# Kernel optimization log

Measured on AMD Instinct MI355X. Metric: run time of the kernel, lower is better.

## Reference

```python
import jax, jax.numpy as jnp
import numpy as np

T, B, D, H = 1024, 128, 256, 256


def setup_inputs() -> dict:
    key = jax.random.key(0)
    ks = jax.random.split(key, 16)
    s_in = 1.0 / np.sqrt(D + H)  # torch Linear default init scale
    inp = {
        "inputs": jax.random.normal(ks[0], (T, B, D), dtype=jnp.float32),
        "Wf": jax.random.uniform(ks[1], (H, D + H), jnp.float32, -s_in, s_in),
        "bf": jax.random.uniform(ks[2], (H,), jnp.float32, -s_in, s_in),
        "Wi": jax.random.uniform(ks[3], (H, D + H), jnp.float32, -s_in, s_in),
        "bi": jax.random.uniform(ks[4], (H,), jnp.float32, -s_in, s_in),
        "Wg": jax.random.uniform(ks[5], (H, D + H), jnp.float32, -s_in, s_in),
        "bg": jax.random.uniform(ks[6], (H,), jnp.float32, -s_in, s_in),
        "Wo": jax.random.uniform(ks[7], (H, D + H), jnp.float32, -s_in, s_in),
        "bo": jax.random.uniform(ks[8], (H,), jnp.float32, -s_in, s_in),
        # estimator params stacked over the 4 gates (order: f, i, g, o)
        "estW1": jax.random.uniform(ks[9], (4, 8, H), jnp.float32, -1/np.sqrt(H), 1/np.sqrt(H)),
        "estb1": jax.random.uniform(ks[10], (4, 8), jnp.float32, -1/np.sqrt(H), 1/np.sqrt(H)),
        "estW2": jax.random.uniform(ks[11], (4, 4, 8), jnp.float32, -1/np.sqrt(8), 1/np.sqrt(8)),
        "estb2": jax.random.uniform(ks[12], (4, 4), jnp.float32, -1/np.sqrt(8), 1/np.sqrt(8)),
        "estW3": jax.random.uniform(ks[13], (4, 1, 4), jnp.float32, -0.5, 0.5),
        "estb3": jax.random.uniform(ks[14], (4, 1), jnp.float32, -0.5, 0.5),
    }
    return inp


def reference(inputs, Wf, bf, Wi, bi, Wg, bg, Wo, bo,
              estW1, estb1, estW2, estb2, estW3, estb3):
    def est(x, k):
        # tiny MLP: H -> 8 -> 4 -> 1 with tanh/tanh/sigmoid
        h1 = jnp.tanh(x @ estW1[k].T + estb1[k])
        h2 = jnp.tanh(h1 @ estW2[k].T + estb2[k])
        return jax.nn.sigmoid(h2 @ estW3[k].T + estb3[k])  # [B, 1]

    def step(carry, x):
        hx, cx = carry
        comb = jnp.concatenate([x, hx], axis=1)  # [B, D+H]
        f = jax.nn.sigmoid(comb @ Wf.T + bf)
        i = jax.nn.sigmoid(comb @ Wi.T + bi)
        g = jnp.tanh(comb @ Wg.T + bg)
        o = jax.nn.sigmoid(comb @ Wo.T + bo)
        f = f * est(f, 0)
        i = i * est(i, 1)
        g = g * est(g, 2)
        o = o * est(o, 3)
        cx = f * cx + i * g
        hx = o * jnp.tanh(cx)
        return (hx, cx), hx

    hx0 = jnp.zeros((B, H), dtype=inputs.dtype)
    cx0 = jnp.zeros((B, H), dtype=inputs.dtype)
    (hx, cx), stacked = jax.lax.scan(step, (hx0, cx0), inputs)
    return stacked, hx, cx
```

## Files before the change

### kernel.cpp

```cpp
#include <hip/hip_runtime.h>
#include <hip/hip_fp16.h>
#include <math.h>

#define T_STEPS 1024
#define BATCH   128
#define D_IN    256
#define H_DIM   256
#define NCOL    1024
#define CH      16

typedef _Float16 half2_t __attribute__((ext_vector_type(2)));

__device__ __forceinline__ float sigmoidf_(float x) {
    return 1.0f / (1.0f + __expf(-x));
}

__device__ __forceinline__ float tanhf_(float x) {
    float ax = fabsf(x);
    float t = __expf(-2.0f * ax);
    float r = (1.0f - t) / (1.0f + t);
    return copysignf(r, x);
}

__device__ __forceinline__ float dot2f(unsigned int w, unsigned int h, float acc) {
#if __has_builtin(__builtin_amdgcn_fdot2)
    return __builtin_amdgcn_fdot2(__builtin_bit_cast(half2_t, w),
                                  __builtin_bit_cast(half2_t, h), acc, false);
#else
    __half2 wv = *(__half2*)&w, hv = *(__half2*)&h;
    acc = fmaf(__half2float(wv.x), __half2float(hv.x), acc);
    return fmaf(__half2float(wv.y), __half2float(hv.y), acc);
#endif
}

__device__ __forceinline__ unsigned int packh2(float a, float b) {
    __half2 p = __floats2half2_rn(a, b);
    return *(unsigned int*)&p;
}

__device__ __forceinline__ uint4 pack8(const float* p) {
    return make_uint4(packh2(p[0], p[1]), packh2(p[2], p[3]),
                      packh2(p[4], p[5]), packh2(p[6], p[7]));
}

__global__ __launch_bounds__(256) void prep_kernel(
    const float* __restrict__ Wf, const float* __restrict__ Wi,
    const float* __restrict__ Wg, const float* __restrict__ Wo,
    const float* __restrict__ bf, const float* __restrict__ bi,
    const float* __restrict__ bg, const float* __restrict__ bo,
    uint4* __restrict__ WX4, uint4* __restrict__ WH4,
    float* __restrict__ biasc)
{
    int idx = blockIdx.x * 256 + threadIdx.x;
    int m = idx >> 10;
    int j = idx & 1023;
    int g = j >> 8;
    int h = j & 255;
    const float* W = (g == 0) ? Wf : (g == 1) ? Wi : (g == 2) ? Wg : Wo;
    const float* row = W + h * (D_IN + H_DIM);
    WX4[idx] = pack8(row + 8 * m);
    WH4[idx] = pack8(row + D_IN + 8 * m);
    if (idx < NCOL) {
        const float* bb = (g == 0) ? bf : (g == 1) ? bi : (g == 2) ? bg : bo;
        biasc[idx] = bb[h];
    }
}

__global__ __launch_bounds__(1024) void qlstm_kernel(
    const float* __restrict__ x,
    const uint4* __restrict__ WX4,
    const uint4* __restrict__ WH4,
    const float* __restrict__ biasc,
    const float* __restrict__ estW1, const float* __restrict__ estb1,
    const float* __restrict__ estW2, const float* __restrict__ estb2,
    const float* __restrict__ estW3, const float* __restrict__ estb3,
    float* __restrict__ out)
{
    __shared__ __align__(16) __half hxh[H_DIM];
    __shared__ __align__(16) __half hxl[H_DIM];
    __shared__ __align__(16) float gact[NCOL];
    __shared__ float w1[4 * 8 * H_DIM];
    __shared__ float sb1[32];
    __shared__ float sW2[128];
    __shared__ float sb2[16];
    __shared__ float sW3[16];
    __shared__ float sb3[4];
    __shared__ float escale[4];

    const int b    = blockIdx.x;
    const int tid  = threadIdx.x;
    const int w    = tid >> 6;
    const int lane = tid & 63;

    for (int i = tid; i < 4 * 8 * H_DIM; i += 1024) {
        int p = i & 255;
        int base = i & ~255;
        int h = 4 * (p & 63) + (p >> 6);
        w1[i] = estW1[base + h];
    }
    if (tid < 32)  sb1[tid] = estb1[tid];
    if (tid < 128) sW2[tid] = estW2[tid];
    if (tid < 16)  { sb2[tid] = estb2[tid]; sW3[tid] = estW3[tid]; }
    if (tid < 4)   sb3[tid] = estb3[tid];
    if (tid < H_DIM) {
        hxh[tid] = __float2half(0.0f);
        hxl[tid] = __float2half(0.0f);
    }
    float c_reg = 0.0f, h_reg = 0.0f;
    const float b_j = biasc[tid];
    __syncthreads();

    const uint4* hh = (const uint4*)hxh;
    const uint4* hl = (const uint4*)hxl;

    float pacc[CH];

    for (int t0 = 0; t0 < T_STEPS; t0 += CH) {
        #pragma unroll
        for (int s = 0; s < CH; s++) pacc[s] = b_j;
        {
            const float* xb = x + ((size_t)t0 * BATCH + b) * D_IN;
            for (int m = 0; m < 32; m++) {
                uint4 wv = WX4[(m << 10) + tid];
                __half2 q0 = *(__half2*)&wv.x, q1 = *(__half2*)&wv.y;
                __half2 q2 = *(__half2*)&wv.z, q3 = *(__half2*)&wv.w;
                float w0 = __half2float(q0.x), w1f = __half2float(q0.y);
                float w2 = __half2float(q1.x), w3 = __half2float(q1.y);
                float w4 = __half2float(q2.x), w5 = __half2float(q2.y);
                float w6 = __half2float(q3.x), w7 = __half2float(q3.y);
                #pragma unroll
                for (int s = 0; s < CH; s++) {
                    const float* xr = xb + (size_t)s * (BATCH * D_IN) + (m << 3);
                    float4 xa = *(const float4*)xr;
                    float4 xc = *(const float4*)(xr + 4);
                    float a = pacc[s];
                    a = fmaf(w0, xa.x, a); a = fmaf(w1f, xa.y, a);
                    a = fmaf(w2, xa.z, a); a = fmaf(w3, xa.w, a);
                    a = fmaf(w4, xc.x, a); a = fmaf(w5, xc.y, a);
                    a = fmaf(w6, xc.z, a); a = fmaf(w7, xc.w, a);
                    pacc[s] = a;
                }
            }
        }

        #pragma unroll 1
        for (int s = 0; s < CH; s++) {
            const int t = t0 + s;
            float aH = pacc[s], aL = 0.0f;
            #pragma unroll 4
            for (int m = 0; m < 32; m++) {
                uint4 wv = WH4[(m << 10) + tid];
                uint4 hv = hh[m], lv = hl[m];
                aH = dot2f(wv.x, hv.x, aH); aH = dot2f(wv.y, hv.y, aH);
                aH = dot2f(wv.z, hv.z, aH); aH = dot2f(wv.w, hv.w, aH);
                aL = dot2f(wv.x, lv.x, aL); aL = dot2f(wv.y, lv.y, aL);
                aL = dot2f(wv.z, lv.z, aL); aL = dot2f(wv.w, lv.w, aL);
            }
            float acc = aH + aL;

            float v = (tid >= 512 && tid < 768) ? tanhf_(acc) : sigmoidf_(acc);
            gact[tid] = v;
            __syncthreads();

            if (tid < 256) {
                float4 gv = ((const float4*)(gact + (w << 8)))[lane];
                float h1[8];
                #pragma unroll
                for (int j = 0; j < 8; j++) {
                    const float* wr = &w1[(w * 8 + j) * H_DIM];
                    float sacc = fmaf(gv.x, wr[lane],
                                 fmaf(gv.y, wr[lane + 64],
                                 fmaf(gv.z, wr[lane + 128], gv.w * wr[lane + 192])));
                    #pragma unroll
                    for (int m2 = 1; m2 < 64; m2 <<= 1) sacc += __shfl_xor(sacc, m2, 64);
                    h1[j] = tanhf_(sacc + sb1[w * 8 + j]);
                }
                float h2[4];
                #pragma unroll
                for (int j = 0; j < 4; j++) {
                    float sacc = sb2[w * 4 + j];
                    #pragma unroll
                    for (int q = 0; q < 8; q++)
                        sacc = fmaf(h1[q], sW2[w * 32 + j * 8 + q], sacc);
                    h2[j] = tanhf_(sacc);
                }
                float s3 = sb3[w];
                #pragma unroll
                for (int q = 0; q < 4; q++) s3 = fmaf(h2[q], sW3[w * 4 + q], s3);
                if (lane == 0) escale[w] = sigmoidf_(s3);
            }
            __syncthreads();

            if (tid < 256) {
                float f  = gact[tid]       * escale[0];
                float ii = gact[256 + tid] * escale[1];
                float gg = gact[512 + tid] * escale[2];
                float o  = gact[768 + tid] * escale[3];
                c_reg = fmaf(f, c_reg, ii * gg);
                h_reg = o * tanhf_(c_reg);
                __half hi = __float2half_rn(h_reg);
                hxh[tid] = hi;
                hxl[tid] = __float2half_rn(h_reg - __half2float(hi));
                out[((size_t)t * BATCH + b) * H_DIM + tid] = h_reg;
            }
            __syncthreads();
        }
    }

    if (tid < 256) {
        const size_t stacked = (size_t)T_STEPS * BATCH * H_DIM;
        out[stacked + (size_t)b * H_DIM + tid] = h_reg;
        out[stacked + (size_t)BATCH * H_DIM + (size_t)b * H_DIM + tid] = c_reg;
    }
}

extern "C" void kernel_launch(void* const* d_in, const int* in_sizes, int n_in,
                              void* d_out, int out_size, void* d_ws, size_t ws_size,
                              hipStream_t stream) {
    const float* x     = (const float*)d_in[0];
    const float* Wf    = (const float*)d_in[1];
    const float* bf    = (const float*)d_in[2];
    const float* Wi    = (const float*)d_in[3];
    const float* bi    = (const float*)d_in[4];
    const float* Wg    = (const float*)d_in[5];
    const float* bg    = (const float*)d_in[6];
    const float* Wo    = (const float*)d_in[7];
    const float* bo    = (const float*)d_in[8];
    const float* estW1 = (const float*)d_in[9];
    const float* estb1 = (const float*)d_in[10];
    const float* estW2 = (const float*)d_in[11];
    const float* estb2 = (const float*)d_in[12];
    const float* estW3 = (const float*)d_in[13];
    const float* estb3 = (const float*)d_in[14];

    uint4* WX4   = (uint4*)d_ws;
    uint4* WH4   = WX4 + 32768;
    float* biasc = (float*)(WH4 + 32768);

    prep_kernel<<<128, 256, 0, stream>>>(Wf, Wi, Wg, Wo, bf, bi, bg, bo,
                                         WX4, WH4, biasc);
    qlstm_kernel<<<BATCH, 1024, 0, stream>>>(
        x, WX4, WH4, biasc,
        estW1, estb1, estW2, estb2, estW3, estb3, (float*)d_out);
}
```

Baseline: 10.64 ms.

## Keep part of recurrent weights in registers, prefetch the rest, spread estimator across waves

The first 8 of the 32 recurrent weight chunks per thread are now held in registers for the whole sequence. The remaining chunks are loaded in double-buffered groups of four, each issued ahead of the dot products that use it, to hide global-load latency on the serial recurrence path. The estimator's first layer is spread across all 16 waves (two hidden units per wave) instead of 4 waves. The small second and third layers are then recomputed redundantly by every thread that updates the cell. This raises register pressure, with launch bounds hinting 4 waves per SIMD, and adds redundant per-thread estimator math.

```diff
diff --git a/kernel.cpp b/kernel.cpp
--- a/kernel.cpp
+++ b/kernel.cpp
@@ -8,6 +8,7 @@
 #define H_DIM   256
 #define NCOL    1024
 #define CH      16
+#define NPER    8
 
 typedef _Float16 half2_t __attribute__((ext_vector_type(2)));
 
@@ -66,7 +67,16 @@
     }
 }
 
-__global__ __launch_bounds__(1024) void qlstm_kernel(
+#define DOT8(wv, mm)                                                        \
+    do {                                                                    \
+        uint4 hv_ = hh[mm], lv_ = hl[mm];                                   \
+        aH = dot2f((wv).x, hv_.x, aH); aH = dot2f((wv).y, hv_.y, aH);       \
+        aH = dot2f((wv).z, hv_.z, aH); aH = dot2f((wv).w, hv_.w, aH);       \
+        aL = dot2f((wv).x, lv_.x, aL); aL = dot2f((wv).y, lv_.y, aL);       \
+        aL = dot2f((wv).z, lv_.z, aL); aL = dot2f((wv).w, lv_.w, aL);       \
+    } while (0)
+
+__global__ __launch_bounds__(1024, 4) void qlstm_kernel(
     const float* __restrict__ x,
     const uint4* __restrict__ WX4,
     const uint4* __restrict__ WH4,
@@ -85,12 +95,14 @@
     __shared__ float sb2[16];
     __shared__ float sW3[16];
     __shared__ float sb3[4];
-    __shared__ float escale[4];
+    __shared__ float sh1[32];
 
     const int b    = blockIdx.x;
     const int tid  = threadIdx.x;
     const int w    = tid >> 6;
     const int lane = tid & 63;
+    const int g_e  = w >> 2;
+    const int j0   = (w & 3) * 2;
 
     for (int i = tid; i < 4 * 8 * H_DIM; i += 1024) {
         int p = i & 255;
@@ -112,6 +124,11 @@
 
     const uint4* hh = (const uint4*)hxh;
     const uint4* hl = (const uint4*)hxl;
+    const uint4* wcol = WH4 + tid;
+
+    uint4 wper[NPER];
+    #pragma unroll
+    for (int m = 0; m < NPER; m++) wper[m] = wcol[m << 10];
 
     float pacc[CH];
 
@@ -146,56 +163,84 @@
         #pragma unroll 1
         for (int s = 0; s < CH; s++) {
             const int t = t0 + s;
-            float aH = pacc[s], aL = 0.0f;
-            #pragma unroll 4
-            for (int m = 0; m < 32; m++) {
-                uint4 wv = WH4[(m << 10) + tid];
-                uint4 hv = hh[m], lv = hl[m];
-                aH = dot2f(wv.x, hv.x, aH); aH = dot2f(wv.y, hv.y, aH);
-                aH = dot2f(wv.z, hv.z, aH); aH = dot2f(wv.w, hv.w, aH);
-                aL = dot2f(wv.x, lv.x, aL); aL = dot2f(wv.y, lv.y, aL);
-                aL = dot2f(wv.z, lv.z, aL); aL = dot2f(wv.w, lv.w, aL);
-            }
+            float aH = pacc[0], aL = 0.0f;
+            #pragma unroll
+            for (int i = 0; i < CH - 1; i++) pacc[i] = pacc[i + 1];
+
+            uint4 sA[4], sB[4];
+            #pragma unroll
+            for (int i = 0; i < 4; i++) sA[i] = wcol[(NPER + i) << 10];
+            #pragma unroll
+            for (int i = 0; i < 4; i++) sB[i] = wcol[(NPER + 4 + i) << 10];
+
+            #pragma unroll
+            for (int m = 0; m < NPER; m++) DOT8(wper[m], m);
+
+            #pragma unroll
+            for (int i = 0; i < 4; i++) DOT8(sA[i], 8 + i);
+            #pragma unroll
+            for (int i = 0; i < 4; i++) sA[i] = wcol[(16 + i) << 10];
+            #pragma unroll
+            for (int i = 0; i < 4; i++) DOT8(sB[i], 12 + i);
+            #pragma unroll
+            for (int i = 0; i < 4; i++) sB[i] = wcol[(20 + i) << 10];
+            #pragma unroll
+            for (int i = 0; i < 4; i++) DOT8(sA[i], 16 + i);
+            #pragma unroll
+            for (int i = 0; i < 4; i++) sA[i] = wcol[(24 + i) << 10];
+            #pragma unroll
+            for (int i = 0; i < 4; i++) DOT8(sB[i], 20 + i);
+            #pragma unroll
+            for (int i = 0; i < 4; i++) sB[i] = wcol[(28 + i) << 10];
+            #pragma unroll
+            for (int i = 0; i < 4; i++) DOT8(sA[i], 24 + i);
+            #pragma unroll
+            for (int i = 0; i < 4; i++) DOT8(sB[i], 28 + i);
+
             float acc = aH + aL;
 
             float v = (tid >= 512 && tid < 768) ? tanhf_(acc) : sigmoidf_(acc);
             gact[tid] = v;
             __syncthreads();
 
-            if (tid < 256) {
-                float4 gv = ((const float4*)(gact + (w << 8)))[lane];
-                float h1[8];
+            {
+                float4 gv = ((const float4*)(gact + (g_e << 8)))[lane];
                 #pragma unroll
-                for (int j = 0; j < 8; j++) {
-                    const float* wr = &w1[(w * 8 + j) * H_DIM];
-                    float sacc = fmaf(gv.x, wr[lane],
-                                 fmaf(gv.y, wr[lane + 64],
-                                 fmaf(gv.z, wr[lane + 128], gv.w * wr[lane + 192])));
+                for (int jj = 0; jj < 2; jj++) {
+                    const int u = g_e * 8 + j0 + jj;
+                    const float* wr = &w1[u * H_DIM];
+                    float s1 = fmaf(gv.x, wr[lane],
+                               fmaf(gv.y, wr[lane + 64],
+                               fmaf(gv.z, wr[lane + 128], gv.w * wr[lane + 192])));
                     #pragma unroll
-                    for (int m2 = 1; m2 < 64; m2 <<= 1) sacc += __shfl_xor(sacc, m2, 64);
-                    h1[j] = tanhf_(sacc + sb1[w * 8 + j]);
+                    for (int m2 = 1; m2 < 64; m2 <<= 1) s1 += __shfl_xor(s1, m2, 64);
+                    if (lane == 0) sh1[u] = tanhf_(s1 + sb1[u]);
                 }
-                float h2[4];
-                #pragma unroll
-                for (int j = 0; j < 4; j++) {
-                    float sacc = sb2[w * 4 + j];
-                    #pragma unroll
-                    for (int q = 0; q < 8; q++)
-                        sacc = fmaf(h1[q], sW2[w * 32 + j * 8 + q], sacc);
-                    h2[j] = tanhf_(sacc);
-                }
-                float s3 = sb3[w];
-                #pragma unroll
-                for (int q = 0; q < 4; q++) s3 = fmaf(h2[q], sW3[w * 4 + q], s3);
-                if (lane == 0) escale[w] = sigmoidf_(s3);
             }
             __syncthreads();
 
             if (tid < 256) {
-                float f  = gact[tid]       * escale[0];
-                float ii = gact[256 + tid] * escale[1];
-                float gg = gact[512 + tid] * escale[2];
-                float o  = gact[768 + tid] * escale[3];
+                float esc[4];
+                #pragma unroll
+                for (int g = 0; g < 4; g++) {
+                    float h2[4];
+                    #pragma unroll
+                    for (int j = 0; j < 4; j++) {
+                        float s2 = sb2[g * 4 + j];
+                        #pragma unroll
+                        for (int q = 0; q < 8; q++)
+                            s2 = fmaf(sh1[g * 8 + q], sW2[g * 32 + j * 8 + q], s2);
+                        h2[j] = tanhf_(s2);
+                    }
+                    float s3 = sb3[g];
+                    #pragma unroll
+                    for (int q = 0; q < 4; q++) s3 = fmaf(h2[q], sW3[g * 4 + q], s3);
+                    esc[g] = sigmoidf_(s3);
+                }
+                float f  = gact[tid]       * esc[0];
+                float ii = gact[256 + tid] * esc[1];
+                float gg = gact[512 + tid] * esc[2];
+                float o  = gact[768 + tid] * esc[3];
                 c_reg = fmaf(f, c_reg, ii * gg);
                 h_reg = o * tanhf_(c_reg);
                 __half hi = __float2half_rn(h_reg);
```

Measured after the change: 16.22 ms. 1.52x slower.
